# Kernel tuning notes

Hardware: AMD Instinct MI355X
Metric: run time of the kernel (lower is better)

## Reference

```python
import jax, jax.numpy as jnp
import numpy as np

H = 1024
NH = 16
HD = H // NH

def setup_inputs() -> dict:
    key = jax.random.key(0)
    ks = jax.random.split(key, 8)
    s = 1.0 / np.sqrt(H)
    hidden_states = jax.random.normal(ks[0], (2, 2048, H), dtype=jnp.float32)
    attention_mask = jnp.zeros((2, 1, 1, 2048), dtype=jnp.float32)
    Wq = jax.random.uniform(ks[1], (H, H), jnp.float32, -s, s)
    bq = jax.random.uniform(ks[2], (H,), jnp.float32, -s, s)
    Wk = jax.random.uniform(ks[3], (H, H), jnp.float32, -s, s)
    bk = jax.random.uniform(ks[4], (H,), jnp.float32, -s, s)
    Wv = jax.random.uniform(ks[5], (H, H), jnp.float32, -s, s)
    bv = jax.random.uniform(ks[6], (H,), jnp.float32, -s, s)
    return {"hidden_states": hidden_states, "attention_mask": attention_mask,
            "Wq": Wq, "bq": bq, "Wk": Wk, "bk": bk, "Wv": Wv, "bv": bv}

def _split_heads(x):
    B, L, _ = x.shape
    return x.reshape(B, L, NH, HD).transpose(0, 2, 1, 3)  # [B, nh, L, hd]

def reference(hidden_states, attention_mask, Wq, bq, Wk, bk, Wv, bv):
    # QKV projections (nn.Linear: x @ W.T + b)
    Q = _split_heads(hidden_states @ Wq.T + bq)
    K = _split_heads(hidden_states @ Wk.T + bk)
    V = _split_heads(hidden_states @ Wv.T + bv)
    scale = 1.0 / np.sqrt(HD)
    scores = jnp.einsum('bhqd,bhkd->bhqk', Q, K) * scale  # [B, nh, L, L]
    scores = scores + attention_mask
    probs = jax.nn.softmax(scores, axis=-1)  # dropout in eval mode = identity
    context = jnp.einsum('bhqk,bhkd->bhqd', probs, V)
    B, _, L, _ = context.shape
    return context.transpose(0, 2, 1, 3).reshape(B, L, H)
```

## Files before the change

kernel.cpp:

```cpp
#include <hip/hip_runtime.h>
#include <math.h>
#include <stdint.h>

#define H_DIM 1024
#define NH 16
#define HD 64
#define B_DIM 2
#define L_DIM 2048
#define M_TOT (B_DIM * L_DIM)

typedef __bf16 bf16_t;
typedef __bf16 bf16x8 __attribute__((ext_vector_type(8)));
typedef __bf16 bf16x4 __attribute__((ext_vector_type(4)));
typedef float  f32x4  __attribute__((ext_vector_type(4)));

__global__ __launch_bounds__(256)
void cast_all(const float* __restrict__ x,
              const float* __restrict__ Wq, const float* __restrict__ Wk,
              const float* __restrict__ Wv, bf16_t* __restrict__ dst)
{
    const size_t idx = ((size_t)blockIdx.x * 256 + threadIdx.x) * 4;
    const float* src;
    size_t off;
    if (idx < (size_t)M_TOT * H_DIM) { src = x; off = idx; }
    else {
        size_t j = idx - (size_t)M_TOT * H_DIM;
        int z = (int)(j >> 20);
        off = j & ((1u << 20) - 1);
        src = (z == 0) ? Wq : (z == 1) ? Wk : Wv;
    }
    const float4 v = *(const float4*)(src + off);
    bf16x4 o;
    o[0] = (bf16_t)v.x; o[1] = (bf16_t)v.y;
    o[2] = (bf16_t)v.z; o[3] = (bf16_t)v.w;
    *(bf16x4*)(dst + idx) = o;
}

__global__ __launch_bounds__(256)
void qkv_mfma(const bf16_t* __restrict__ xb, const bf16_t* __restrict__ wb,
              const float* __restrict__ bq, const float* __restrict__ bk,
              const float* __restrict__ bv,
              bf16_t* __restrict__ qb, bf16_t* __restrict__ kb,
              bf16_t* __restrict__ vt)
{
    __shared__ bf16_t As[128 * 32];
    __shared__ bf16_t Bs[128 * 32];

    const int tid  = threadIdx.x;
    const int z    = blockIdx.z;
    const int bm   = blockIdx.x * 128;
    const int bn   = blockIdx.y * 128;
    const bf16_t* W    = wb + (size_t)z * H_DIM * H_DIM;
    const float*  bias = (z == 0) ? bq : (z == 1) ? bk : bv;

    const int wave = tid >> 6;
    const int lane = tid & 63;
    const int lc   = lane & 15;
    const int quad = lane >> 4;
    const int wm   = wave >> 1;
    const int wn   = wave & 1;

    f32x4 acc[4][4];
    #pragma unroll
    for (int i = 0; i < 4; ++i)
        #pragma unroll
        for (int j = 0; j < 4; ++j)
            acc[i][j] = (f32x4){0.f, 0.f, 0.f, 0.f};

    const int srow = tid >> 2;
    const int sseg = tid & 3;
    const bf16_t* gA = xb + (size_t)(bm + srow) * H_DIM + sseg * 8;
    const bf16_t* gB = W  + (size_t)(bn + srow) * H_DIM + sseg * 8;
    char* ldsA = (char*)As + (tid >> 6) * 1024;
    char* ldsB = (char*)Bs + (tid >> 6) * 1024;

    for (int k0 = 0; k0 < H_DIM; k0 += 32) {
        __syncthreads();
        __builtin_amdgcn_global_load_lds(
            (const __attribute__((address_space(1))) void*)(gA + k0),
            (__attribute__((address_space(3))) void*)ldsA, 16, 0, 0);
        __builtin_amdgcn_global_load_lds(
            (const __attribute__((address_space(1))) void*)(gA + k0 + (size_t)64 * H_DIM),
            (__attribute__((address_space(3))) void*)(ldsA + 4096), 16, 0, 0);
        __builtin_amdgcn_global_load_lds(
            (const __attribute__((address_space(1))) void*)(gB + k0),
            (__attribute__((address_space(3))) void*)ldsB, 16, 0, 0);
        __builtin_amdgcn_global_load_lds(
            (const __attribute__((address_space(1))) void*)(gB + k0 + (size_t)64 * H_DIM),
            (__attribute__((address_space(3))) void*)(ldsB + 4096), 16, 0, 0);
        __syncthreads();

        bf16x8 a[4], b[4];
        #pragma unroll
        for (int mi = 0; mi < 4; ++mi)
            a[mi] = *(const bf16x8*)(As + (wm * 64 + mi * 16 + lc) * 32 + quad * 8);
        #pragma unroll
        for (int ni = 0; ni < 4; ++ni)
            b[ni] = *(const bf16x8*)(Bs + (wn * 64 + ni * 16 + lc) * 32 + quad * 8);
        #pragma unroll
        for (int mi = 0; mi < 4; ++mi)
            #pragma unroll
            for (int ni = 0; ni < 4; ++ni)
                acc[mi][ni] = __builtin_amdgcn_mfma_f32_16x16x32_bf16(
                    a[mi], b[ni], acc[mi][ni], 0, 0, 0);
    }

    const int nb = bn + wn * 64;
    float biasv[4];
    #pragma unroll
    for (int ni = 0; ni < 4; ++ni) biasv[ni] = bias[nb + ni * 16 + lc];

    #pragma unroll
    for (int mi = 0; mi < 4; ++mi) {
        const int m0 = bm + wm * 64 + mi * 16 + quad * 4;
        if (z == 2) {
            const int b_ = m0 >> 11;
            const int l0 = m0 & 2047;
            #pragma unroll
            for (int ni = 0; ni < 4; ++ni) {
                const int n = nb + ni * 16 + lc;
                const int h = n >> 6, d = n & 63;
                bf16x4 pk;
                #pragma unroll
                for (int r = 0; r < 4; ++r)
                    pk[r] = (bf16_t)(acc[mi][ni][r] + biasv[ni]);
                *(bf16x4*)(vt + (((size_t)(b_ * NH + h)) * HD + d) * L_DIM + l0) = pk;
            }
        } else {
            bf16_t* dst = (z == 0) ? qb : kb;
            #pragma unroll
            for (int r = 0; r < 4; ++r) {
                const int m  = m0 + r;
                const int b_ = m >> 11;
                const int l  = m & 2047;
                #pragma unroll
                for (int ni = 0; ni < 4; ++ni) {
                    const int n = nb + ni * 16 + lc;
                    const int h = n >> 6, d = n & 63;
                    dst[(((size_t)(b_ * NH + h)) * L_DIM + l) * HD + d] =
                        (bf16_t)(acc[mi][ni][r] + biasv[ni]);
                }
            }
        }
    }
}

#define EXP_C   0.180336879f
#define LOG2E   1.442695041f
#define EXP_SH  11.541560327f

__device__ __forceinline__ void attn_tile(
    int kbase, bool pre,
    const bf16_t* curK, const bf16_t* curV,
    bf16_t* nxtK, bf16_t* nxtV,
    const bf16_t* gK, const bf16_t* gV,
    bf16_t* Pbuf, const float* mrow, int lc, int quad,
    const bf16x8 (&bQ)[2][2], f32x4 (&o)[2][4], float (&rs)[2])
{
    __builtin_amdgcn_s_waitcnt(0x0F70);

    bf16x8 kf[4][2], vf[4][2];
    #pragma unroll
    for (int ni = 0; ni < 4; ++ni) {
        const bf16_t* p = curK + (ni * 16 + lc) * 64 + quad * 8;
        kf[ni][0] = *(const bf16x8*)p;
        kf[ni][1] = *(const bf16x8*)(p + 32);
    }
    #pragma unroll
    for (int dg = 0; dg < 4; ++dg) {
        const bf16_t* p = curV + (dg * 16 + lc) * 64 + quad * 8;
        vf[dg][0] = *(const bf16x8*)p;
        vf[dg][1] = *(const bf16x8*)(p + 32);
    }

    if (pre) {
        const int nk = kbase + 64;
        #pragma unroll
        for (int i = 0; i < 8; ++i) {
            __builtin_amdgcn_global_load_lds(
                (const __attribute__((address_space(1))) void*)(gK + (size_t)nk * 64 + i * 512),
                (__attribute__((address_space(3))) void*)(nxtK + i * 512), 16, 0, 0);
            __builtin_amdgcn_global_load_lds(
                (const __attribute__((address_space(1))) void*)(gV + nk + i * 16384),
                (__attribute__((address_space(3))) void*)(nxtV + i * 512), 16, 0, 0);
        }
    }

    float mvs[4][4];
    #pragma unroll
    for (int ni = 0; ni < 4; ++ni) {
        const float4 mv = *(const float4*)(mrow + kbase + ni * 16 + quad * 4);
        mvs[ni][0] = mv.x * LOG2E - EXP_SH;
        mvs[ni][1] = mv.y * LOG2E - EXP_SH;
        mvs[ni][2] = mv.z * LOG2E - EXP_SH;
        mvs[ni][3] = mv.w * LOG2E - EXP_SH;
    }

    f32x4 s[2][4];
    #pragma unroll
    for (int f = 0; f < 2; ++f)
        #pragma unroll
        for (int ni = 0; ni < 4; ++ni) {
            f32x4 t = (f32x4){0.f, 0.f, 0.f, 0.f};
            t = __builtin_amdgcn_mfma_f32_16x16x32_bf16(kf[ni][0], bQ[f][0], t, 0, 0, 0);
            t = __builtin_amdgcn_mfma_f32_16x16x32_bf16(kf[ni][1], bQ[f][1], t, 0, 0, 0);
            s[f][ni] = t;
        }

    #pragma unroll
    for (int f = 0; f < 2; ++f) {
        bf16_t* buf = Pbuf + f * 1152;
        float acc = 0.f;
        #pragma unroll
        for (int ni = 0; ni < 4; ++ni) {
            bf16x4 pk;
            #pragma unroll
            for (int r = 0; r < 4; ++r) {
                const float p = __builtin_amdgcn_exp2f(s[f][ni][r] * EXP_C + mvs[ni][r]);
                acc += p;
                pk[r] = (bf16_t)p;
            }
            *(bf16x4*)(buf + lc * 72 + ni * 16 + quad * 4) = pk;
        }
        rs[f] += acc;
    }

    #pragma unroll
    for (int f = 0; f < 2; ++f) {
        const bf16_t* buf = Pbuf + f * 1152;
        const bf16x8 bP0 = *(const bf16x8*)(buf + lc * 72 + quad * 8);
        const bf16x8 bP1 = *(const bf16x8*)(buf + lc * 72 + 32 + quad * 8);
        #pragma unroll
        for (int dg = 0; dg < 4; ++dg) {
            o[f][dg] = __builtin_amdgcn_mfma_f32_16x16x32_bf16(vf[dg][0], bP0, o[f][dg], 0, 0, 0);
            o[f][dg] = __builtin_amdgcn_mfma_f32_16x16x32_bf16(vf[dg][1], bP1, o[f][dg], 0, 0, 0);
        }
    }
}

__global__ __launch_bounds__(64, 1)
void attn_mfma(const bf16_t* __restrict__ qb, const bf16_t* __restrict__ kb,
               const bf16_t* __restrict__ vt, const float* __restrict__ mask,
               float* __restrict__ out)
{
    __shared__ bf16_t Ks0[64 * 64];
    __shared__ bf16_t Ks1[64 * 64];
    __shared__ bf16_t Vs0[64 * 64];
    __shared__ bf16_t Vs1[64 * 64];
    __shared__ bf16_t Ps[2 * 16 * 72];

    const int lane = threadIdx.x & 63;
    const int lc   = lane & 15;
    const int quad = lane >> 4;
    const int rl   = lane >> 3;
    const int sg   = lane & 7;
    const int bh   = blockIdx.x;
    const int b_   = bh >> 4;
    const int h    = bh & 15;
    const int q0   = blockIdx.y * 32;

    bf16x8 bQ[2][2];
    #pragma unroll
    for (int f = 0; f < 2; ++f) {
        const bf16_t* Qp = qb + ((size_t)bh * L_DIM + q0 + f * 16 + lc) * HD + quad * 8;
        bQ[f][0] = *(const bf16x8*)(Qp);
        bQ[f][1] = *(const bf16x8*)(Qp + 32);
    }

    const bf16_t* Kbase = kb + (size_t)bh * L_DIM * HD;
    const bf16_t* Vbase = vt + (size_t)bh * HD * L_DIM;
    const float*  mrow  = mask + (size_t)b_ * L_DIM;

    const bf16_t* gK = Kbase + rl * 64 + sg * 8;
    const bf16_t* gV = Vbase + (size_t)rl * 2048 + sg * 8;

    f32x4 o[2][4];
    #pragma unroll
    for (int f = 0; f < 2; ++f)
        #pragma unroll
        for (int dg = 0; dg < 4; ++dg) o[f][dg] = (f32x4){0.f, 0.f, 0.f, 0.f};
    float rs[2] = {0.f, 0.f};

    #pragma unroll
    for (int i = 0; i < 8; ++i) {
        __builtin_amdgcn_global_load_lds(
            (const __attribute__((address_space(1))) void*)(gK + i * 512),
            (__attribute__((address_space(3))) void*)(Ks0 + i * 512), 16, 0, 0);
        __builtin_amdgcn_global_load_lds(
            (const __attribute__((address_space(1))) void*)(gV + i * 16384),
            (__attribute__((address_space(3))) void*)(Vs0 + i * 512), 16, 0, 0);
    }

    #pragma unroll 1
    for (int t2 = 0; t2 < 16; ++t2) {
        const int kb0 = t2 * 128;
        attn_tile(kb0,      true,     Ks0, Vs0, Ks1, Vs1, gK, gV, Ps,
                  mrow, lc, quad, bQ, o, rs);
        attn_tile(kb0 + 64, t2 < 15,  Ks1, Vs1, Ks0, Vs0, gK, gV, Ps,
                  mrow, lc, quad, bQ, o, rs);
    }

    #pragma unroll
    for (int f = 0; f < 2; ++f) {
        float l = rs[f];
        l += __shfl_xor(l, 16);
        l += __shfl_xor(l, 32);
        const float inv = 1.0f / l;
        float* orow = out + ((size_t)(b_ * L_DIM + q0 + f * 16 + lc)) * H_DIM
                    + h * HD + quad * 4;
        #pragma unroll
        for (int dg = 0; dg < 4; ++dg) {
            f32x4 w = o[f][dg];
            w[0] *= inv; w[1] *= inv; w[2] *= inv; w[3] *= inv;
            *(f32x4*)(orow + dg * 16) = w;
        }
    }
}

extern "C" void kernel_launch(void* const* d_in, const int* in_sizes, int n_in,
                              void* d_out, int out_size, void* d_ws, size_t ws_size,
                              hipStream_t stream) {
    const float* hidden = (const float*)d_in[0];
    const float* mask   = (const float*)d_in[1];
    const float* Wq     = (const float*)d_in[2];
    const float* bq     = (const float*)d_in[3];
    const float* Wk     = (const float*)d_in[4];
    const float* bk     = (const float*)d_in[5];
    const float* Wv     = (const float*)d_in[6];
    const float* bv     = (const float*)d_in[7];
    float* out = (float*)d_out;

    const size_t XN = (size_t)M_TOT * H_DIM;
    const size_t WN = (size_t)3 * H_DIM * H_DIM;
    bf16_t* xwb = (bf16_t*)d_ws;
    bf16_t* qb  = xwb + XN + WN;
    bf16_t* kb  = qb + XN;
    bf16_t* vt  = kb + XN;

    cast_all<<<(int)((XN + WN) / 1024), 256, 0, stream>>>(hidden, Wq, Wk, Wv, xwb);

    dim3 g1(M_TOT / 128, H_DIM / 128, 3);
    qkv_mfma<<<g1, 256, 0, stream>>>(xwb, xwb + XN, bq, bk, bv, qb, kb, vt);

    dim3 g2(B_DIM * NH, L_DIM / 32);
    attn_mfma<<<g2, 64, 0, stream>>>(qb, kb, vt, mask, out);
}
```

Before: 210.9 us.

## Double query rows per attention wave and XOR-swizzle K/V/P shared memory

Each single-wave attention block now handles 64 query rows instead of 32, so every K/V tile loaded into shared memory feeds twice as many MFMAs. The grid is halved to match. K, V and P buffers in shared memory switch to an XOR swizzle keyed on row (replacing the padded P stride) to avoid LDS bank conflicts, and V fragment loads move after the softmax to lower register pressure. The cost is more accumulator registers and only 1024 single-wave blocks, which reduces occupancy and latency hiding.

```diff
diff --git a/kernel.cpp b/kernel.cpp
--- a/kernel.cpp
+++ b/kernel.cpp
@@ -154,23 +154,17 @@
     const bf16_t* curK, const bf16_t* curV,
     bf16_t* nxtK, bf16_t* nxtV,
     const bf16_t* gK, const bf16_t* gV,
-    bf16_t* Pbuf, const float* mrow, int lc, int quad,
-    const bf16x8 (&bQ)[2][2], f32x4 (&o)[2][4], float (&rs)[2])
+    bf16_t* Ps, const float* mrow, int lc, int quad, int e,
+    const bf16x8 (&bQ)[4][2], f32x4 (&o)[4][4], float (&rs)[4])
 {
     __builtin_amdgcn_s_waitcnt(0x0F70);
 
-    bf16x8 kf[4][2], vf[4][2];
+    bf16x8 kf[4][2];
     #pragma unroll
     for (int ni = 0; ni < 4; ++ni) {
-        const bf16_t* p = curK + (ni * 16 + lc) * 64 + quad * 8;
-        kf[ni][0] = *(const bf16x8*)p;
-        kf[ni][1] = *(const bf16x8*)(p + 32);
-    }
-    #pragma unroll
-    for (int dg = 0; dg < 4; ++dg) {
-        const bf16_t* p = curV + (dg * 16 + lc) * 64 + quad * 8;
-        vf[dg][0] = *(const bf16x8*)p;
-        vf[dg][1] = *(const bf16x8*)(p + 32);
+        const bf16_t* p = curK + (ni * 16 + lc) * 64;
+        kf[ni][0] = *(const bf16x8*)(p + (quad ^ e) * 8);
+        kf[ni][1] = *(const bf16x8*)(p + ((quad ^ e) ^ 4) * 8);
     }
 
     if (pre) {
@@ -178,7 +172,7 @@
         #pragma unroll
         for (int i = 0; i < 8; ++i) {
             __builtin_amdgcn_global_load_lds(
-                (const __attribute__((address_space(1))) void*)(gK + (size_t)nk * 64 + i * 512),
+                (const __attribute__((address_space(1))) void*)(gK + nk * 64 + i * 512),
                 (__attribute__((address_space(3))) void*)(nxtK + i * 512), 16, 0, 0);
             __builtin_amdgcn_global_load_lds(
                 (const __attribute__((address_space(1))) void*)(gV + nk + i * 16384),
@@ -196,40 +190,46 @@
         mvs[ni][3] = mv.w * LOG2E - EXP_SH;
     }
 
-    f32x4 s[2][4];
-    #pragma unroll
-    for (int f = 0; f < 2; ++f)
+    #pragma unroll
+    for (int f = 0; f < 4; ++f) {
+        f32x4 s[4];
         #pragma unroll
         for (int ni = 0; ni < 4; ++ni) {
             f32x4 t = (f32x4){0.f, 0.f, 0.f, 0.f};
             t = __builtin_amdgcn_mfma_f32_16x16x32_bf16(kf[ni][0], bQ[f][0], t, 0, 0, 0);
             t = __builtin_amdgcn_mfma_f32_16x16x32_bf16(kf[ni][1], bQ[f][1], t, 0, 0, 0);
-            s[f][ni] = t;
-        }
-
-    #pragma unroll
-    for (int f = 0; f < 2; ++f) {
-        bf16_t* buf = Pbuf + f * 1152;
+            s[ni] = t;
+        }
+        bf16_t* buf = Ps + f * 1024;
         float acc = 0.f;
         #pragma unroll
         for (int ni = 0; ni < 4; ++ni) {
             bf16x4 pk;
             #pragma unroll
             for (int r = 0; r < 4; ++r) {
-                const float p = __builtin_amdgcn_exp2f(s[f][ni][r] * EXP_C + mvs[ni][r]);
+                const float p = __builtin_amdgcn_exp2f(s[ni][r] * EXP_C + mvs[ni][r]);
                 acc += p;
                 pk[r] = (bf16_t)p;
             }
-            *(bf16x4*)(buf + lc * 72 + ni * 16 + quad * 4) = pk;
+            *(bf16x4*)(buf + lc * 64 + (((ni * 2 + (quad >> 1)) ^ e) * 8)
+                       + ((quad & 1) * 4)) = pk;
         }
         rs[f] += acc;
     }
 
-    #pragma unroll
-    for (int f = 0; f < 2; ++f) {
-        const bf16_t* buf = Pbuf + f * 1152;
-        const bf16x8 bP0 = *(const bf16x8*)(buf + lc * 72 + quad * 8);
-        const bf16x8 bP1 = *(const bf16x8*)(buf + lc * 72 + 32 + quad * 8);
+    bf16x8 vf[4][2];
+    #pragma unroll
+    for (int dg = 0; dg < 4; ++dg) {
+        const bf16_t* p = curV + (dg * 16 + lc) * 64;
+        vf[dg][0] = *(const bf16x8*)(p + (quad ^ e) * 8);
+        vf[dg][1] = *(const bf16x8*)(p + ((quad ^ e) ^ 4) * 8);
+    }
+
+    #pragma unroll
+    for (int f = 0; f < 4; ++f) {
+        const bf16_t* buf = Ps + f * 1024;
+        const bf16x8 bP0 = *(const bf16x8*)(buf + lc * 64 + (quad ^ e) * 8);
+        const bf16x8 bP1 = *(const bf16x8*)(buf + lc * 64 + ((quad ^ e) ^ 4) * 8);
         #pragma unroll
         for (int dg = 0; dg < 4; ++dg) {
             o[f][dg] = __builtin_amdgcn_mfma_f32_16x16x32_bf16(vf[dg][0], bP0, o[f][dg], 0, 0, 0);
@@ -247,21 +247,22 @@
     __shared__ bf16_t Ks1[64 * 64];
     __shared__ bf16_t Vs0[64 * 64];
     __shared__ bf16_t Vs1[64 * 64];
-    __shared__ bf16_t Ps[2 * 16 * 72];
+    __shared__ bf16_t Ps[4 * 16 * 64];
 
     const int lane = threadIdx.x & 63;
     const int lc   = lane & 15;
     const int quad = lane >> 4;
+    const int e    = lc & 7;
     const int rl   = lane >> 3;
     const int sg   = lane & 7;
     const int bh   = blockIdx.x;
     const int b_   = bh >> 4;
     const int h    = bh & 15;
-    const int q0   = blockIdx.y * 32;
-
-    bf16x8 bQ[2][2];
-    #pragma unroll
-    for (int f = 0; f < 2; ++f) {
+    const int q0   = blockIdx.y * 64;
+
+    bf16x8 bQ[4][2];
+    #pragma unroll
+    for (int f = 0; f < 4; ++f) {
         const bf16_t* Qp = qb + ((size_t)bh * L_DIM + q0 + f * 16 + lc) * HD + quad * 8;
         bQ[f][0] = *(const bf16x8*)(Qp);
         bQ[f][1] = *(const bf16x8*)(Qp + 32);
@@ -271,15 +272,15 @@
     const bf16_t* Vbase = vt + (size_t)bh * HD * L_DIM;
     const float*  mrow  = mask + (size_t)b_ * L_DIM;
 
-    const bf16_t* gK = Kbase + rl * 64 + sg * 8;
-    const bf16_t* gV = Vbase + (size_t)rl * 2048 + sg * 8;
-
-    f32x4 o[2][4];
-    #pragma unroll
-    for (int f = 0; f < 2; ++f)
+    const bf16_t* gK = Kbase + rl * 64 + (sg ^ rl) * 8;
+    const bf16_t* gV = Vbase + (size_t)rl * 2048 + (sg ^ rl) * 8;
+
+    f32x4 o[4][4];
+    #pragma unroll
+    for (int f = 0; f < 4; ++f)
         #pragma unroll
         for (int dg = 0; dg < 4; ++dg) o[f][dg] = (f32x4){0.f, 0.f, 0.f, 0.f};
-    float rs[2] = {0.f, 0.f};
+    float rs[4] = {0.f, 0.f, 0.f, 0.f};
 
     #pragma unroll
     for (int i = 0; i < 8; ++i) {
@@ -294,14 +295,14 @@
     #pragma unroll 1
     for (int t2 = 0; t2 < 16; ++t2) {
         const int kb0 = t2 * 128;
-        attn_tile(kb0,      true,     Ks0, Vs0, Ks1, Vs1, gK, gV, Ps,
-                  mrow, lc, quad, bQ, o, rs);
-        attn_tile(kb0 + 64, t2 < 15,  Ks1, Vs1, Ks0, Vs0, gK, gV, Ps,
-                  mrow, lc, quad, bQ, o, rs);
-    }
-
-    #pragma unroll
-    for (int f = 0; f < 2; ++f) {
+        attn_tile(kb0,      true,    Ks0, Vs0, Ks1, Vs1, gK, gV, Ps,
+                  mrow, lc, quad, e, bQ, o, rs);
+        attn_tile(kb0 + 64, t2 < 15, Ks1, Vs1, Ks0, Vs0, gK, gV, Ps,
+                  mrow, lc, quad, e, bQ, o, rs);
+    }
+
+    #pragma unroll
+    for (int f = 0; f < 4; ++f) {
         float l = rs[f];
         l += __shfl_xor(l, 16);
         l += __shfl_xor(l, 32);
@@ -342,6 +343,6 @@
     dim3 g1(M_TOT / 128, H_DIM / 128, 3);
     qkv_mfma<<<g1, 256, 0, stream>>>(xwb, xwb + XN, bq, bk, bv, qb, kb, vt);
 
-    dim3 g2(B_DIM * NH, L_DIM / 32);
+    dim3 g2(B_DIM * NH, L_DIM / 64);
     attn_mfma<<<g2, 64, 0, stream>>>(qb, kb, vt, mask, out);
 }
```

New measurement: 199.5 us. -5.4%, faster.

## Double-buffer QKV GEMM, swizzle LDS, shrink attention key tile for occupancy

Applied to the files above, without the earlier changes.

The QKV projection GEMM now ping-pongs between two LDS buffers, so the next K-slice loads while MFMAs run on the current one, and the LDS layout is XOR-swizzled to avoid bank conflicts. The attention kernel shrinks its key/value tile from 64 to 32 keys and swizzles the K, V and P layouts, cutting LDS and register use so launch bounds can allow two blocks per CU. The trade-off is twice as many attention loop iterations and more waitcnt/sync overhead per key processed.

```diff
diff --git a/kernel.cpp b/kernel.cpp
--- a/kernel.cpp
+++ b/kernel.cpp
@@ -13,6 +13,9 @@
 typedef __bf16 bf16x8 __attribute__((ext_vector_type(8)));
 typedef __bf16 bf16x4 __attribute__((ext_vector_type(4)));
 typedef float  f32x4  __attribute__((ext_vector_type(4)));
+
+#define AS1 const __attribute__((address_space(1))) void*
+#define AS3 __attribute__((address_space(3))) void*
 
 __global__ __launch_bounds__(256)
 void cast_all(const float* __restrict__ x,
@@ -43,8 +46,10 @@
               bf16_t* __restrict__ qb, bf16_t* __restrict__ kb,
               bf16_t* __restrict__ vt)
 {
-    __shared__ bf16_t As[128 * 32];
-    __shared__ bf16_t Bs[128 * 32];
+    __shared__ bf16_t As0[128 * 32];
+    __shared__ bf16_t Bs0[128 * 32];
+    __shared__ bf16_t As1[128 * 32];
+    __shared__ bf16_t Bs1[128 * 32];
 
     const int tid  = threadIdx.x;
     const int z    = blockIdx.z;
@@ -69,40 +74,48 @@
 
     const int srow = tid >> 2;
     const int sseg = tid & 3;
-    const bf16_t* gA = xb + (size_t)(bm + srow) * H_DIM + sseg * 8;
-    const bf16_t* gB = W  + (size_t)(bn + srow) * H_DIM + sseg * 8;
-    char* ldsA = (char*)As + (tid >> 6) * 1024;
-    char* ldsB = (char*)Bs + (tid >> 6) * 1024;
-
-    for (int k0 = 0; k0 < H_DIM; k0 += 32) {
-        __syncthreads();
-        __builtin_amdgcn_global_load_lds(
-            (const __attribute__((address_space(1))) void*)(gA + k0),
-            (__attribute__((address_space(3))) void*)ldsA, 16, 0, 0);
-        __builtin_amdgcn_global_load_lds(
-            (const __attribute__((address_space(1))) void*)(gA + k0 + (size_t)64 * H_DIM),
-            (__attribute__((address_space(3))) void*)(ldsA + 4096), 16, 0, 0);
-        __builtin_amdgcn_global_load_lds(
-            (const __attribute__((address_space(1))) void*)(gB + k0),
-            (__attribute__((address_space(3))) void*)ldsB, 16, 0, 0);
-        __builtin_amdgcn_global_load_lds(
-            (const __attribute__((address_space(1))) void*)(gB + k0 + (size_t)64 * H_DIM),
-            (__attribute__((address_space(3))) void*)(ldsB + 4096), 16, 0, 0);
-        __syncthreads();
-
+    const bf16_t* gA = xb + (size_t)(bm + srow) * H_DIM + (sseg ^ (srow & 3)) * 8;
+    const bf16_t* gB = W  + (size_t)(bn + srow) * H_DIM + (sseg ^ (srow & 3)) * 8;
+    const int woff = wave * 1024;
+
+    auto stage = [&](int k0, bf16_t* A_, bf16_t* B_) {
+        __builtin_amdgcn_global_load_lds((AS1)(gA + k0),
+            (AS3)((char*)A_ + woff), 16, 0, 0);
+        __builtin_amdgcn_global_load_lds((AS1)(gA + k0 + (size_t)64 * H_DIM),
+            (AS3)((char*)A_ + woff + 4096), 16, 0, 0);
+        __builtin_amdgcn_global_load_lds((AS1)(gB + k0),
+            (AS3)((char*)B_ + woff), 16, 0, 0);
+        __builtin_amdgcn_global_load_lds((AS1)(gB + k0 + (size_t)64 * H_DIM),
+            (AS3)((char*)B_ + woff + 4096), 16, 0, 0);
+    };
+
+    const int slot = (quad ^ (lc & 3)) * 8;
+    auto compute = [&](const bf16_t* A_, const bf16_t* B_) {
         bf16x8 a[4], b[4];
         #pragma unroll
         for (int mi = 0; mi < 4; ++mi)
-            a[mi] = *(const bf16x8*)(As + (wm * 64 + mi * 16 + lc) * 32 + quad * 8);
+            a[mi] = *(const bf16x8*)(A_ + (wm * 64 + mi * 16 + lc) * 32 + slot);
         #pragma unroll
         for (int ni = 0; ni < 4; ++ni)
-            b[ni] = *(const bf16x8*)(Bs + (wn * 64 + ni * 16 + lc) * 32 + quad * 8);
+            b[ni] = *(const bf16x8*)(B_ + (wn * 64 + ni * 16 + lc) * 32 + slot);
         #pragma unroll
         for (int mi = 0; mi < 4; ++mi)
             #pragma unroll
             for (int ni = 0; ni < 4; ++ni)
                 acc[mi][ni] = __builtin_amdgcn_mfma_f32_16x16x32_bf16(
                     a[mi], b[ni], acc[mi][ni], 0, 0, 0);
+    };
+
+    stage(0, As0, Bs0);
+    #pragma unroll 1
+    for (int kk = 0; kk < 16; ++kk) {
+        const int k0 = kk * 64;
+        __syncthreads();
+        stage(k0 + 32, As1, Bs1);
+        compute(As0, Bs0);
+        __syncthreads();
+        if (k0 + 64 < H_DIM) stage(k0 + 64, As0, Bs0);
+        compute(As1, Bs1);
     }
 
     const int nb = bn + wn * 64;
@@ -149,46 +162,43 @@
 #define LOG2E   1.442695041f
 #define EXP_SH  11.541560327f
 
-__device__ __forceinline__ void attn_tile(
+__device__ __forceinline__ void attn_tile32(
     int kbase, bool pre,
     const bf16_t* curK, const bf16_t* curV,
     bf16_t* nxtK, bf16_t* nxtV,
     const bf16_t* gK, const bf16_t* gV,
-    bf16_t* Pbuf, const float* mrow, int lc, int quad,
+    bf16_t* Ps, const float* mrow, int lc, int quad,
     const bf16x8 (&bQ)[2][2], f32x4 (&o)[2][4], float (&rs)[2])
 {
     __builtin_amdgcn_s_waitcnt(0x0F70);
 
-    bf16x8 kf[4][2], vf[4][2];
-    #pragma unroll
-    for (int ni = 0; ni < 4; ++ni) {
-        const bf16_t* p = curK + (ni * 16 + lc) * 64 + quad * 8;
-        kf[ni][0] = *(const bf16x8*)p;
-        kf[ni][1] = *(const bf16x8*)(p + 32);
-    }
-    #pragma unroll
-    for (int dg = 0; dg < 4; ++dg) {
-        const bf16_t* p = curV + (dg * 16 + lc) * 64 + quad * 8;
-        vf[dg][0] = *(const bf16x8*)p;
-        vf[dg][1] = *(const bf16x8*)(p + 32);
+    const int e  = lc & 7;
+    const int e3 = lc & 3;
+
+    bf16x8 kf[2][2];
+    #pragma unroll
+    for (int ni = 0; ni < 2; ++ni) {
+        const bf16_t* p = curK + (ni * 16 + lc) * 64;
+        kf[ni][0] = *(const bf16x8*)(p + ((quad ^ e) << 3));
+        kf[ni][1] = *(const bf16x8*)(p + (((quad ^ e) ^ 4) << 3));
     }
 
     if (pre) {
-        const int nk = kbase + 64;
-        #pragma unroll
-        for (int i = 0; i < 8; ++i) {
+        const int nk = kbase + 32;
+        #pragma unroll
+        for (int i = 0; i < 4; ++i) {
             __builtin_amdgcn_global_load_lds(
-                (const __attribute__((address_space(1))) void*)(gK + (size_t)nk * 64 + i * 512),
-                (__attribute__((address_space(3))) void*)(nxtK + i * 512), 16, 0, 0);
+                (AS1)(gK + (size_t)nk * 64 + i * 512),
+                (AS3)(nxtK + i * 512), 16, 0, 0);
             __builtin_amdgcn_global_load_lds(
-                (const __attribute__((address_space(1))) void*)(gV + nk + i * 16384),
-                (__attribute__((address_space(3))) void*)(nxtV + i * 512), 16, 0, 0);
-        }
-    }
-
-    float mvs[4][4];
-    #pragma unroll
-    for (int ni = 0; ni < 4; ++ni) {
+                (AS1)(gV + nk + i * 32768),
+                (AS3)(nxtV + i * 512), 16, 0, 0);
+        }
+    }
+
+    float mvs[2][4];
+    #pragma unroll
+    for (int ni = 0; ni < 2; ++ni) {
         const float4 mv = *(const float4*)(mrow + kbase + ni * 16 + quad * 4);
         mvs[ni][0] = mv.x * LOG2E - EXP_SH;
         mvs[ni][1] = mv.y * LOG2E - EXP_SH;
@@ -196,58 +206,61 @@
         mvs[ni][3] = mv.w * LOG2E - EXP_SH;
     }
 
-    f32x4 s[2][4];
-    #pragma unroll
-    for (int f = 0; f < 2; ++f)
-        #pragma unroll
-        for (int ni = 0; ni < 4; ++ni) {
+    #pragma unroll
+    for (int f = 0; f < 2; ++f) {
+        f32x4 s[2];
+        #pragma unroll
+        for (int ni = 0; ni < 2; ++ni) {
             f32x4 t = (f32x4){0.f, 0.f, 0.f, 0.f};
             t = __builtin_amdgcn_mfma_f32_16x16x32_bf16(kf[ni][0], bQ[f][0], t, 0, 0, 0);
             t = __builtin_amdgcn_mfma_f32_16x16x32_bf16(kf[ni][1], bQ[f][1], t, 0, 0, 0);
-            s[f][ni] = t;
-        }
-
-    #pragma unroll
-    for (int f = 0; f < 2; ++f) {
-        bf16_t* buf = Pbuf + f * 1152;
+            s[ni] = t;
+        }
+        bf16_t* buf = Ps + f * 512;
         float acc = 0.f;
         #pragma unroll
-        for (int ni = 0; ni < 4; ++ni) {
+        for (int ni = 0; ni < 2; ++ni) {
             bf16x4 pk;
             #pragma unroll
             for (int r = 0; r < 4; ++r) {
-                const float p = __builtin_amdgcn_exp2f(s[f][ni][r] * EXP_C + mvs[ni][r]);
+                const float p = __builtin_amdgcn_exp2f(s[ni][r] * EXP_C + mvs[ni][r]);
                 acc += p;
                 pk[r] = (bf16_t)p;
             }
-            *(bf16x4*)(buf + lc * 72 + ni * 16 + quad * 4) = pk;
+            *(bf16x4*)(buf + lc * 32 + (((ni * 2 + (quad >> 1)) ^ e3) << 3)
+                       + ((quad & 1) << 2)) = pk;
         }
         rs[f] += acc;
     }
 
+    bf16x8 vf[4];
+    const int e2 = lc >> 1;
+    #pragma unroll
+    for (int dg = 0; dg < 4; ++dg) {
+        const int p  = dg * 8 + (lc >> 1);
+        const int ch = (((lc & 1) << 2) + quad) ^ e2;
+        vf[dg] = *(const bf16x8*)(curV + p * 64 + (ch << 3));
+    }
+
     #pragma unroll
     for (int f = 0; f < 2; ++f) {
-        const bf16_t* buf = Pbuf + f * 1152;
-        const bf16x8 bP0 = *(const bf16x8*)(buf + lc * 72 + quad * 8);
-        const bf16x8 bP1 = *(const bf16x8*)(buf + lc * 72 + 32 + quad * 8);
-        #pragma unroll
-        for (int dg = 0; dg < 4; ++dg) {
-            o[f][dg] = __builtin_amdgcn_mfma_f32_16x16x32_bf16(vf[dg][0], bP0, o[f][dg], 0, 0, 0);
-            o[f][dg] = __builtin_amdgcn_mfma_f32_16x16x32_bf16(vf[dg][1], bP1, o[f][dg], 0, 0, 0);
-        }
-    }
-}
-
-__global__ __launch_bounds__(64, 1)
+        const bf16x8 bP = *(const bf16x8*)(Ps + f * 512 + lc * 32 + ((quad ^ e3) << 3));
+        #pragma unroll
+        for (int dg = 0; dg < 4; ++dg)
+            o[f][dg] = __builtin_amdgcn_mfma_f32_16x16x32_bf16(vf[dg], bP, o[f][dg], 0, 0, 0);
+    }
+}
+
+__global__ __launch_bounds__(64, 2)
 void attn_mfma(const bf16_t* __restrict__ qb, const bf16_t* __restrict__ kb,
                const bf16_t* __restrict__ vt, const float* __restrict__ mask,
                float* __restrict__ out)
 {
-    __shared__ bf16_t Ks0[64 * 64];
-    __shared__ bf16_t Ks1[64 * 64];
-    __shared__ bf16_t Vs0[64 * 64];
-    __shared__ bf16_t Vs1[64 * 64];
-    __shared__ bf16_t Ps[2 * 16 * 72];
+    __shared__ bf16_t Ks0[32 * 64];
+    __shared__ bf16_t Ks1[32 * 64];
+    __shared__ bf16_t Vs0[32 * 64];
+    __shared__ bf16_t Vs1[32 * 64];
+    __shared__ bf16_t Ps[2 * 16 * 32];
 
     const int lane = threadIdx.x & 63;
     const int lc   = lane & 15;
@@ -271,8 +284,11 @@
     const bf16_t* Vbase = vt + (size_t)bh * HD * L_DIM;
     const float*  mrow  = mask + (size_t)b_ * L_DIM;
 
-    const bf16_t* gK = Kbase + rl * 64 + sg * 8;
-    const bf16_t* gV = Vbase + (size_t)rl * 2048 + sg * 8;
+    const bf16_t* gK = Kbase + rl * 64 + (sg ^ rl) * 8;
+    {
+    }
+    const int cV = sg ^ rl;
+    const bf16_t* gV = Vbase + (size_t)(rl * 2 + (cV >> 2)) * L_DIM + (cV & 3) * 8;
 
     f32x4 o[2][4];
     #pragma unroll
@@ -282,22 +298,22 @@
     float rs[2] = {0.f, 0.f};
 
     #pragma unroll
-    for (int i = 0; i < 8; ++i) {
+    for (int i = 0; i < 4; ++i) {
         __builtin_amdgcn_global_load_lds(
-            (const __attribute__((address_space(1))) void*)(gK + i * 512),
-            (__attribute__((address_space(3))) void*)(Ks0 + i * 512), 16, 0, 0);
+            (AS1)(gK + i * 512),
+            (AS3)(Ks0 + i * 512), 16, 0, 0);
         __builtin_amdgcn_global_load_lds(
-            (const __attribute__((address_space(1))) void*)(gV + i * 16384),
-            (__attribute__((address_space(3))) void*)(Vs0 + i * 512), 16, 0, 0);
+            (AS1)(gV + i * 32768),
+            (AS3)(Vs0 + i * 512), 16, 0, 0);
     }
 
     #pragma unroll 1
-    for (int t2 = 0; t2 < 16; ++t2) {
-        const int kb0 = t2 * 128;
-        attn_tile(kb0,      true,     Ks0, Vs0, Ks1, Vs1, gK, gV, Ps,
-                  mrow, lc, quad, bQ, o, rs);
-        attn_tile(kb0 + 64, t2 < 15,  Ks1, Vs1, Ks0, Vs0, gK, gV, Ps,
-                  mrow, lc, quad, bQ, o, rs);
+    for (int t2 = 0; t2 < 32; ++t2) {
+        const int kb0 = t2 * 64;
+        attn_tile32(kb0,      true,     Ks0, Vs0, Ks1, Vs1, gK, gV, Ps,
+                    mrow, lc, quad, bQ, o, rs);
+        attn_tile32(kb0 + 32, t2 < 31,  Ks1, Vs1, Ks0, Vs0, gK, gV, Ps,
+                    mrow, lc, quad, bQ, o, rs);
     }
 
     #pragma unroll
```

New measurement: 188.5 us. 10.6% less time.
